# Performance work log

Hardware: AMD Instinct MI355X
Metric: run time of the kernel (lower is better)

The kernel has to match this reference:

```python
import jax, jax.numpy as jnp
import numpy as np
import math

D_MODEL = 1024
N_HEAD = 16          # sub-heads per branch
N_BR = 4             # hardcoded n_branches
DH = D_MODEL // N_HEAD
H_TOT = N_BR * N_HEAD
B, T = 1, 1024
SCALE = math.pi / math.sqrt(3.0)
ATTNSCALE = DH ** -0.5


def _rope(x):
    # x: [B, H, T, D]; matches torch RoPE: even/odd split, concat halves
    t_len, d = x.shape[2], x.shape[-1]
    inv_freq = 1.0 / (10000.0 ** (jnp.arange(0, d, 2, dtype=jnp.float32) / d))
    freqs = jnp.arange(t_len, dtype=jnp.float32)[:, None] * inv_freq[None, :]  # [T, D/2]
    cos, sin = jnp.cos(freqs), jnp.sin(freqs)
    x1, x2 = x[..., 0::2], x[..., 1::2]
    return jnp.concatenate([-x2 * sin + x1 * cos, x1 * sin + x2 * cos], axis=-1)


def setup_inputs() -> dict:
    key = jax.random.key(0)
    ks = jax.random.split(key, 12)
    s = D_MODEL ** -0.5
    return {
        "X": jax.random.normal(ks[0], (B, T, D_MODEL), jnp.float32),
        "W_Q": jax.random.normal(ks[1], (D_MODEL, D_MODEL * N_BR), jnp.float32) * s,
        "b_Q": jax.random.normal(ks[2], (D_MODEL * N_BR,), jnp.float32) * 0.02,
        "W_K": jax.random.normal(ks[3], (D_MODEL, D_MODEL), jnp.float32) * s,
        "b_K": jax.random.normal(ks[4], (D_MODEL,), jnp.float32) * 0.02,
        "W_V": jax.random.normal(ks[5], (D_MODEL, D_MODEL), jnp.float32) * s,
        "b_V": jax.random.normal(ks[6], (D_MODEL,), jnp.float32) * 0.02,
        "sink_scalars": jax.random.uniform(ks[7], (H_TOT,), jnp.float32, 0.0, 0.1),
        "v_nulls": jax.random.normal(ks[8], (N_BR, D_MODEL), jnp.float32) * 0.02,
        "W_O": jax.random.normal(ks[9], (N_BR, D_MODEL, D_MODEL), jnp.float32) * s,
        "W_O_bias": jax.random.normal(ks[10], (N_BR, D_MODEL), jnp.float32) * 0.02,
    }


def reference(X, W_Q, b_Q, W_K, b_K, W_V, b_V, sink_scalars, v_nulls, W_O, W_O_bias):
    Bv, Tv, C = X.shape
    # projections -> [B, H, T, Dh]
    q = (X @ W_Q + b_Q).reshape(Bv, Tv, H_TOT, DH).transpose(0, 2, 1, 3)
    k_base = (X @ W_K + b_K).reshape(Bv, Tv, N_HEAD, DH).transpose(0, 2, 1, 3)
    v_base = (X @ W_V + b_V).reshape(Bv, Tv, N_HEAD, DH).transpose(0, 2, 1, 3)
    k = jnp.tile(k_base, (1, N_BR, 1, 1))
    v = jnp.tile(v_base, (1, N_BR, 1, 1))
    q, k = _rope(q), _rope(k)

    scores = jnp.einsum("bhtd,bhsd->bhts", q, k) * ATTNSCALE
    key_self = jnp.clip(jnp.sum(k * k, axis=-1), 1e-6, None)      # [B,H,S]
    w = jax.nn.softplus(scores / jnp.sqrt(key_self)[:, :, None, :])
    causal = jnp.tril(jnp.ones((Tv, Tv), bool))                    # [T,S]
    w = jnp.where(causal, w, 0.0)
    w = w * jax.nn.sigmoid(SCALE * w)
    sinks = sink_scalars.reshape(1, H_TOT, 1, 1)
    w = jnp.where(w < sinks, 0.0, w)
    # concat-with-sink renormalization, expressed without the concat
    total = jnp.sum(w, axis=-1, keepdims=True) + sinks + 1e-6      # [B,H,T,1]
    probs_tokens = w / total
    probs_sink = sinks / total                                     # [B,H,T,1]

    out = jnp.einsum("bhts,bhsd->bhtd", probs_tokens, v)
    v_null = v_nulls.reshape(H_TOT, DH)[None, :, None, :]          # [1,H,1,Dh]
    out = out + probs_sink * v_null

    context = out.reshape(Bv, N_BR, N_HEAD, Tv, DH).transpose(0, 1, 3, 2, 4)
    context = context.reshape(Bv, N_BR, Tv, C)
    y = jnp.einsum("bntc,ncd->bntd", context, W_O) + W_O_bias[None, :, None, :]
    return y.mean(axis=1)
```

## Files before the change

kernel.cpp:

```cpp
#include <hip/hip_runtime.h>
#include <math.h>

typedef __attribute__((ext_vector_type(4))) float  f32x4;
typedef __attribute__((ext_vector_type(8))) short  bf16x8;
typedef __attribute__((ext_vector_type(4))) short  s16x4;

#define SQUISH_U 1.8137993642342178f
#define LN2F     0.69314718055994531f

__device__ __forceinline__ float b2f(short u) {
    union { float f; unsigned b; } v; v.b = ((unsigned)(unsigned short)u) << 16; return v.f;
}
__device__ __forceinline__ short f2b(float f) {
    union { float f; unsigned b; } v; v.f = f;
    unsigned r = (v.b + 0x7FFFu + ((v.b >> 16) & 1u)) >> 16;
    return (short)r;
}
__device__ __forceinline__ unsigned cvt_pk_bf16(float lo, float hi) {
    unsigned r;
    asm("v_cvt_pk_bf16_f32 %0, %1, %2" : "=v"(r) : "v"(lo), "v"(hi));
    return r;
}
__device__ __forceinline__ void gll16(const void* g, void* l) {
    __builtin_amdgcn_global_load_lds((const __attribute__((address_space(1))) void*)g,
                                     (__attribute__((address_space(3))) void*)l, 16, 0, 0);
}
__device__ __forceinline__ void gll4(const void* g, void* l) {
    __builtin_amdgcn_global_load_lds((const __attribute__((address_space(1))) void*)g,
                                     (__attribute__((address_space(3))) void*)l, 4, 0, 0);
}

__device__ __forceinline__ void do_transpose(const float* __restrict__ src, int R, int C,
                                             short* __restrict__ dst, float scale,
                                             int c0, int r0, float (*tile)[65], int tid) {
    #pragma unroll
    for (int it = 0; it < 4; ++it) {
        int lin = it * 256 + tid;
        int r = lin >> 4, c4 = lin & 15;
        f32x4 v = *(const f32x4*)(src + (size_t)(r0 + r) * C + c0 + c4 * 4);
        #pragma unroll
        for (int k = 0; k < 4; ++k) tile[r][c4 * 4 + k] = v[k];
    }
    __syncthreads();
    #pragma unroll
    for (int it = 0; it < 4; ++it) {
        int lin = it * 256 + tid;
        int c = lin >> 4, rq = lin & 15;
        s16x4 o;
        #pragma unroll
        for (int k = 0; k < 4; ++k) o[k] = f2b(tile[rq * 4 + k][c] * scale);
        *(s16x4*)(dst + (size_t)(c0 + c) * R + r0 + rq * 4) = o;
    }
}

__global__ __launch_bounds__(256) void prep_kernel(
    const float* __restrict__ X, const float* __restrict__ W_Q, const float* __restrict__ W_K,
    const float* __restrict__ W_V, const float* __restrict__ W_O,
    const float* __restrict__ bQ, const float* __restrict__ bK, const float* __restrict__ bV,
    const float* __restrict__ bO,
    short* __restrict__ Xb, short* __restrict__ WbT, short* __restrict__ WoT,
    float* __restrict__ biasQKV, float* __restrict__ out) {
    __shared__ float tile[64][65];
    const int bid = blockIdx.x, tid = threadIdx.x;
    if (bid < 256) {
        int i = (bid * 256 + tid) * 16;
        #pragma unroll
        for (int k = 0; k < 4; ++k) {
            f32x4 v = *(const f32x4*)(X + i + k * 4);
            s16x4 o;
            o.x = f2b(v.x); o.y = f2b(v.y); o.z = f2b(v.z); o.w = f2b(v.w);
            *(s16x4*)(Xb + i + k * 4) = o;
        }
    } else if (bid < 1280) {
        int b2 = bid - 256;
        do_transpose(W_Q, 1024, 4096, WbT, 1.f, (b2 & 63) * 64, (b2 >> 6) * 64, tile, tid);
    } else if (bid < 1536) {
        int b2 = bid - 1280;
        do_transpose(W_K, 1024, 1024, WbT + 4096 * 1024, 1.f, (b2 & 15) * 64, (b2 >> 4) * 64, tile, tid);
    } else if (bid < 1792) {
        int b2 = bid - 1536;
        do_transpose(W_V, 1024, 1024, WbT + 5120 * 1024, 1.f, (b2 & 15) * 64, (b2 >> 4) * 64, tile, tid);
    } else if (bid < 2816) {
        int b2 = bid - 1792;
        do_transpose(W_O, 4096, 1024, WoT, 0.25f, (b2 & 15) * 64, (b2 >> 4) * 64, tile, tid);
    } else if (bid < 2840) {
        int i = (bid - 2816) * 256 + tid;
        if (i < 4096)      biasQKV[i] = bQ[i];
        else if (i < 5120) biasQKV[i] = bK[i - 4096];
        else               biasQKV[i] = bV[i - 5120];
    } else {
        int i = ((bid - 2840) * 256 + tid) * 4;
        f32x4 v;
        #pragma unroll
        for (int k = 0; k < 4; ++k) {
            int c = (i + k) & 1023;
            v[k] = 0.25f * (bO[c] + bO[1024 + c] + bO[2048 + c] + bO[3072 + c]);
        }
        *(f32x4*)(out + i) = v;
    }
}

#define GSTAGE_64x128(k0_, b_) do {                                            \
    _Pragma("unroll")                                                          \
    for (int it = 0; it < 2; ++it) {                                           \
        int lin0 = it * 256 + wave * 64;                                       \
        int lin = lin0 + lane;                                                 \
        int r = lin >> 3, c = (lin & 7) ^ (r & 7);                             \
        gll16(A + (size_t)(m0 + r) * K + (k0_) + c * 8, (char*)lA[b_] + lin0 * 16); \
    }                                                                          \
    _Pragma("unroll")                                                          \
    for (int it = 0; it < 4; ++it) {                                           \
        int lin0 = it * 256 + wave * 64;                                       \
        int lin = lin0 + lane;                                                 \
        int r = lin >> 3, c = (lin & 7) ^ (r & 7);                             \
        gll16(BT + (size_t)(n0 + r) * K + (k0_) + c * 8, (char*)lB[b_] + lin0 * 16); \
    } } while (0)

#define GEMM_CORE_64x128(kbeg_, kend_)                                         \
    GSTAGE_64x128(kbeg_, 0);                                                   \
    int cur = 0;                                                               \
    for (int k0 = (kbeg_); k0 < (kend_); k0 += 64) {                           \
        if (k0 + 64 < (kend_)) {                                               \
            GSTAGE_64x128(k0 + 64, cur ^ 1);                                   \
            asm volatile("s_waitcnt vmcnt(6) lgkmcnt(0)" ::: "memory");        \
        } else {                                                               \
            asm volatile("s_waitcnt vmcnt(0) lgkmcnt(0)" ::: "memory");        \
        }                                                                      \
        __builtin_amdgcn_s_barrier();                                          \
        _Pragma("unroll")                                                      \
        for (int kk = 0; kk < 2; ++kk) {                                       \
            bf16x8 af[2], bf_[4];                                              \
            _Pragma("unroll")                                                  \
            for (int m = 0; m < 2; ++m) {                                      \
                int row = wr * 32 + m * 16 + l15;                              \
                int ch = (kk * 4 + l4) ^ (row & 7);                            \
                af[m] = *(const bf16x8*)&lA[cur][row][ch << 3];                \
            }                                                                  \
            _Pragma("unroll")                                                  \
            for (int n = 0; n < 4; ++n) {                                      \
                int row = wc * 64 + n * 16 + l15;                              \
                int ch = (kk * 4 + l4) ^ (row & 7);                            \
                bf_[n] = *(const bf16x8*)&lB[cur][row][ch << 3];               \
            }                                                                  \
            _Pragma("unroll")                                                  \
            for (int m = 0; m < 2; ++m)                                        \
                _Pragma("unroll")                                              \
                for (int n = 0; n < 4; ++n)                                    \
                    acc[m][n] = __builtin_amdgcn_mfma_f32_16x16x32_bf16(af[m], bf_[n], acc[m][n], 0, 0, 0); \
        }                                                                      \
        asm volatile("" ::: "memory");                                         \
        __builtin_amdgcn_s_barrier();                                          \
        cur ^= 1;                                                              \
    }

__global__ __launch_bounds__(256, 3) void gemm_qkv_kernel(
    const short* __restrict__ A, const short* __restrict__ BT,
    const float* __restrict__ bias, short* __restrict__ outB,
    int M, int N, int K) {
    __shared__ short lA[2][64][64];
    __shared__ short lB[2][128][64];
    const int tid = threadIdx.x;
    const int lane = tid & 63, wave = tid >> 6;
    const int l15 = lane & 15, l4 = lane >> 4;
    const int wr = wave >> 1, wc = wave & 1;
    const int n0 = blockIdx.x * 128, m0 = blockIdx.y * 64;

    f32x4 acc[2][4];
    const f32x4 fz = {0.f, 0.f, 0.f, 0.f};
    #pragma unroll
    for (int m = 0; m < 2; ++m)
        #pragma unroll
        for (int n = 0; n < 4; ++n) acc[m][n] = fz;

    GEMM_CORE_64x128(0, K);

    #pragma unroll
    for (int m = 0; m < 2; ++m)
        #pragma unroll
        for (int n = 0; n < 4; ++n)
            #pragma unroll
            for (int r = 0; r < 4; ++r) {
                int row = m0 + wr * 32 + m * 16 + l4 * 4 + r;
                int col = n0 + wc * 64 + n * 16 + l15;
                outB[(size_t)row * N + col] = f2b(acc[m][n][r] + bias[col]);
            }
}

__global__ __launch_bounds__(256, 3) void gemm_op_kernel(
    const short* __restrict__ A, const short* __restrict__ BT,
    float* __restrict__ out, int M, int N, int K, int KSLICE) {
    __shared__ short lA[2][64][64];
    __shared__ short lB[2][128][64];
    const int tid = threadIdx.x;
    const int lane = tid & 63, wave = tid >> 6;
    const int l15 = lane & 15, l4 = lane >> 4;
    const int wr = wave >> 1, wc = wave & 1;
    const int n0 = blockIdx.x * 128, m0 = blockIdx.y * 64;
    const int kbeg = blockIdx.z * KSLICE, kend = kbeg + KSLICE;

    f32x4 acc[2][4];
    const f32x4 fz = {0.f, 0.f, 0.f, 0.f};
    #pragma unroll
    for (int m = 0; m < 2; ++m)
        #pragma unroll
        for (int n = 0; n < 4; ++n) acc[m][n] = fz;

    GEMM_CORE_64x128(kbeg, kend);

    #pragma unroll
    for (int m = 0; m < 2; ++m)
        #pragma unroll
        for (int n = 0; n < 4; ++n)
            #pragma unroll
            for (int r = 0; r < 4; ++r) {
                int row = m0 + wr * 32 + m * 16 + l4 * 4 + r;
                int col = n0 + wc * 64 + n * 16 + l15;
                unsafeAtomicAdd(&out[(size_t)row * N + col], acc[m][n][r]);
            }
}

__global__ __launch_bounds__(256) void rope_vt_kernel(short* __restrict__ QKVb,
                                                      float* __restrict__ ksr,
                                                      short* __restrict__ Vtb) {
    __shared__ short tile[64][72];
    const int bid = blockIdx.x, tid = threadIdx.x;
    if (bid < 1280) {
        int base = bid * 256 + tid;
        #pragma unroll
        for (int it = 0; it < 8; ++it) {
            int item = base + it * 327680;
            int j = item & 31;
            int rem = item >> 5;
            int head = rem % 80;
            int t = rem / 80;
            short* p;
            if (head < 64) p = QKVb + (size_t)t * 6144 + head * 64;
            else           p = QKVb + (size_t)t * 6144 + 4096 + (head - 64) * 64;
            float x1 = b2f(p[2 * j]), x2 = b2f(p[2 * j + 1]);
            float freq = (float)t * __builtin_exp2f(-(float)j * 0.41524101186092033f);
            float sn = __sinf(freq), cs = __cosf(freq);
            float o1 = x1 * cs - x2 * sn;
            float o2 = x1 * sn + x2 * cs;
            p[j]      = f2b(o1);
            p[32 + j] = f2b(o2);
            if (head >= 64) {
                float ss = o1 * o1 + o2 * o2;
                #pragma unroll
                for (int off = 16; off; off >>= 1) ss += __shfl_xor(ss, off, 32);
                if (j == 0) ksr[(head - 64) * 1024 + t] = 0.18033688011112042f * rsqrtf(fmaxf(ss, 1e-6f));
            }
        }
    } else {
        int b2 = bid - 1280;
        int h = b2 >> 4, t0 = (b2 & 15) * 64;
        #pragma unroll
        for (int it = 0; it < 16; ++it) {
            int lin = it * 256 + tid;
            int r = lin >> 6, d = lin & 63;
            tile[r][d] = QKVb[(size_t)(t0 + r) * 6144 + 5120 + h * 64 + d];
        }
        __syncthreads();
        #pragma unroll
        for (int it = 0; it < 16; ++it) {
            int lin = it * 256 + tid;
            int d = lin >> 6, c = lin & 63;
            Vtb[(size_t)(h * 64 + d) * 1024 + t0 + c] = tile[c][d];
        }
    }
}

__constant__ __device__ const signed char TQT[24] = {15,15,14, 7,14,13,13,12, 6,12,11,11,10, 5,10, 9, 9, 8, 4, 8, 3, 2, 1, 0};
__constant__ __device__ const signed char TKB[24] = { 0, 8, 0, 0, 8, 0, 7, 0, 0, 7, 0, 6, 0, 0, 6, 0, 5, 0, 0, 5, 0, 0, 0, 0};
__constant__ __device__ const signed char TKE[24] = { 8,16, 8, 8,15, 7,14, 7, 7,13, 6,12, 6, 6,11, 5,10, 5, 5, 9, 4, 3, 2, 1};

__global__ __launch_bounds__(256, 6) void attn_kernel(
    const short* __restrict__ QKVb, const short* __restrict__ Vtb,
    const float* __restrict__ ksr, const float* __restrict__ sinks,
    const float* __restrict__ vnulls, short* __restrict__ Ob,
    float* __restrict__ Of, float* __restrict__ totf) {
    __shared__ short lK[64][64];
    __shared__ short lV[64][64];
    __shared__ float lks[64];
    __shared__ float lvn[64];
    __shared__ short lP[4][16][64];

    const int tid = threadIdx.x;
    const int lane = tid & 63, wave = tid >> 6;
    const int l15 = lane & 15, l4 = lane >> 4;
    const int h = blockIdx.x;
    const int slot = blockIdx.y;
    const int qt = TQT[slot], kb = TKB[slot], ke = TKE[slot];
    const bool single = (kb == 0) && (ke == qt + 1);
    const int h16 = h & 15;
    const int t0 = qt * 64;
    const float sink = sinks[h];
    if (tid < 64) lvn[tid] = vnulls[h * 64 + tid];

    const int q_abs = t0 + wave * 16 + l15;
    bf16x8 aq[2];
    #pragma unroll
    for (int kk = 0; kk < 2; ++kk)
        aq[kk] = *(const bf16x8*)(QKVb + (size_t)q_abs * 6144 + h * 64 + kk * 32 + l4 * 8);

    const f32x4 fz = {0.f, 0.f, 0.f, 0.f};
    f32x4 acc_o[4];
    #pragma unroll
    for (int n = 0; n < 4; ++n) acc_o[n] = fz;
    float tot = 0.f;

#define ASTAGE(s0_) do {                                                              \
    int lin0 = wave * 64;                                                             \
    int lin = lin0 + lane;                                                            \
    int r = lin >> 3, c = (lin & 7) ^ (r & 7);                                        \
    gll16(QKVb + (size_t)((s0_) + r) * 6144 + 4096 + h16 * 64 + c * 8, (char*)lK + lin0 * 16); \
    gll16(Vtb + (size_t)(h16 * 64 + r) * 1024 + (s0_) + c * 8,         (char*)lV + lin0 * 16); \
    lin0 += 256; lin = lin0 + lane; r = lin >> 3; c = (lin & 7) ^ (r & 7);            \
    gll16(QKVb + (size_t)((s0_) + r) * 6144 + 4096 + h16 * 64 + c * 8, (char*)lK + lin0 * 16); \
    gll16(Vtb + (size_t)(h16 * 64 + r) * 1024 + (s0_) + c * 8,         (char*)lV + lin0 * 16); \
    gll4(ksr + h16 * 1024 + (s0_) + lane, (char*)lks);                                \
} while (0)

    for (int kt = kb; kt < ke; ++kt) {
        int s0 = kt * 64;
        __syncthreads();
        ASTAGE(s0);
        asm volatile("s_waitcnt vmcnt(0)" ::: "memory");
        __syncthreads();

        f32x4 accs[4];
        #pragma unroll
        for (int n = 0; n < 4; ++n) accs[n] = fz;
        #pragma unroll
        for (int kk = 0; kk < 2; ++kk) {
            bf16x8 bk[4];
            #pragma unroll
            for (int n = 0; n < 4; ++n) {
                int row = n * 16 + l15;
                int ch = (kk * 4 + l4) ^ (row & 7);
                bk[n] = *(const bf16x8*)&lK[row][ch << 3];
            }
            #pragma unroll
            for (int n = 0; n < 4; ++n)
                accs[n] = __builtin_amdgcn_mfma_f32_16x16x32_bf16(bk[n], aq[kk], accs[n], 0, 0, 0);
        }

        #pragma unroll
        for (int n = 0; n < 4; ++n) {
            f32x4 ksv = *(const f32x4*)&lks[n * 16 + l4 * 4];
            float w4[4];
            #pragma unroll
            for (int r = 0; r < 4; ++r) {
                int k_abs = s0 + n * 16 + l4 * 4 + r;
                float zz = accs[n][r] * ksv[r];
                float t = __builtin_amdgcn_exp2f(zz);
                float u = __builtin_amdgcn_logf(1.f + t);
                u = (k_abs <= q_abs) ? u : 0.f;
                float g = __builtin_amdgcn_rcpf(1.f + __builtin_amdgcn_exp2f(-SQUISH_U * u));
                float w = LN2F * u * g;
                w = (w >= sink) ? w : 0.f;
                tot += w;
                w4[r] = w;
            }
            unsigned pa = cvt_pk_bf16(w4[0], w4[1]);
            unsigned pb = cvt_pk_bf16(w4[2], w4[3]);
            int ch = (2 * n + (l4 >> 1)) ^ (l15 & 7);
            uint2 val; val.x = pa; val.y = pb;
            *(uint2*)&lP[wave][l15][ch * 8 + (l4 & 1) * 4] = val;
        }

        #pragma unroll
        for (int kk = 0; kk < 2; ++kk) {
            bf16x8 ap = *(const bf16x8*)&lP[wave][l15][((kk * 4 + l4) ^ (l15 & 7)) << 3];
            bf16x8 bv[4];
            #pragma unroll
            for (int n = 0; n < 4; ++n) {
                int row = n * 16 + l15;
                int ch = (kk * 4 + l4) ^ (row & 7);
                bv[n] = *(const bf16x8*)&lV[row][ch << 3];
            }
            #pragma unroll
            for (int n = 0; n < 4; ++n)
                acc_o[n] = __builtin_amdgcn_mfma_f32_16x16x32_bf16(ap, bv[n], acc_o[n], 0, 0, 0);
        }
    }
#undef ASTAGE

    tot += __shfl_xor(tot, 16, 64);
    tot += __shfl_xor(tot, 32, 64);

    if (single) {
        float tq[4];
        #pragma unroll
        for (int r = 0; r < 4; ++r) tq[r] = __shfl(tot, l4 * 4 + r, 64);
        #pragma unroll
        for (int r = 0; r < 4; ++r) {
            float inv = __builtin_amdgcn_rcpf(tq[r] + sink + 1e-6f);
            int trow = t0 + wave * 16 + l4 * 4 + r;
            #pragma unroll
            for (int n = 0; n < 4; ++n) {
                int d = n * 16 + l15;
                float val = (acc_o[n][r] + sink * lvn[d]) * inv;
                Ob[(size_t)trow * 4096 + h * 64 + d] = f2b(val);
            }
        }
    } else {
        if (lane < 16)
            unsafeAtomicAdd(&totf[h * 512 + (t0 - 512) + wave * 16 + l15], tot);
        #pragma unroll
        for (int r = 0; r < 4; ++r) {
            int pr = h * 512 + (t0 - 512) + wave * 16 + l4 * 4 + r;
            #pragma unroll
            for (int n = 0; n < 4; ++n)
                unsafeAtomicAdd(&Of[(size_t)pr * 64 + n * 16 + l15], acc_o[n][r]);
        }
    }
}

__global__ __launch_bounds__(256) void norm_kernel(
    const float* __restrict__ Of, const float* __restrict__ totf,
    const float* __restrict__ sinks, const float* __restrict__ vnulls,
    short* __restrict__ Ob) {
    int gid = blockIdx.x * 256 + threadIdx.x;
    int i4 = gid * 4;
    int row = i4 >> 6;
    int d0 = i4 & 63;
    int h = row >> 9;
    int t = 512 + (row & 511);
    float sink = sinks[h];
    float inv = __builtin_amdgcn_rcpf(totf[row] + sink + 1e-6f);
    f32x4 o = *(const f32x4*)(Of + i4);
    s16x4 rs;
    #pragma unroll
    for (int k = 0; k < 4; ++k)
        rs[k] = f2b((o[k] + sink * vnulls[h * 64 + d0 + k]) * inv);
    *(s16x4*)(Ob + (size_t)t * 4096 + h * 64 + d0) = rs;
}

extern "C" void kernel_launch(void* const* d_in, const int* in_sizes, int n_in,
                              void* d_out, int out_size, void* d_ws, size_t ws_size,
                              hipStream_t stream) {
    const float* X        = (const float*)d_in[0];
    const float* W_Q      = (const float*)d_in[1];
    const float* b_Q      = (const float*)d_in[2];
    const float* W_K      = (const float*)d_in[3];
    const float* b_K      = (const float*)d_in[4];
    const float* W_V      = (const float*)d_in[5];
    const float* b_V      = (const float*)d_in[6];
    const float* sinks    = (const float*)d_in[7];
    const float* v_nulls  = (const float*)d_in[8];
    const float* W_O      = (const float*)d_in[9];
    const float* W_O_bias = (const float*)d_in[10];
    float* out = (float*)d_out;
    char* ws = (char*)d_ws;

    short* Xb        = (short*)(ws + 0);
    short* WbT       = (short*)(ws + 2097152);
    short* WoT       = (short*)(ws + 14680064);
    short* QKVb      = (short*)(ws + 23068672);
    short* Vtb       = (short*)(ws + 35651584);
    short* Ob        = (short*)(ws + 37748736);
    float* ksr       = (float*)(ws + 46137344);
    float* biasQKV   = (float*)(ws + 46202880);
    float* Of        = (float*)(ws + 2097152);
    float* totf      = Of + 64 * 512 * 64;

    prep_kernel<<<3864, 256, 0, stream>>>(X, W_Q, W_K, W_V, W_O, b_Q, b_K, b_V, W_O_bias,
                                          Xb, WbT, WoT, biasQKV, out);
    gemm_qkv_kernel<<<dim3(48, 16), 256, 0, stream>>>(Xb, WbT, biasQKV, QKVb, 1024, 6144, 1024);
    rope_vt_kernel<<<1536, 256, 0, stream>>>(QKVb, ksr, Vtb);
    hipMemsetAsync(Of, 0, (size_t)(64 * 512 * 64 + 64 * 512) * sizeof(float), stream);
    attn_kernel<<<dim3(64, 24), 256, 0, stream>>>(QKVb, Vtb, ksr, sinks, v_nulls, Ob, Of, totf);
    norm_kernel<<<2048, 256, 0, stream>>>(Of, totf, sinks, v_nulls, Ob);
    gemm_op_kernel<<<dim3(8, 16, 8), 256, 0, stream>>>(Ob, WoT, out, 1024, 1024, 4096, 512);
}
```

Measured before the change: 204.7 us.

## Fuse RoPE, key norms and V transpose into QKV GEMM epilogue; drop atomics

Moves RoPE, the key self-norm and the V transpose into the QKV GEMM epilogue, using lane shuffles within each 16-lane group to pair even and odd columns. This removes the separate rope_vt kernel and its extra read-modify-write pass over QKV. Attention split-K partials are now written to two separate buffers with plain stores instead of atomics, so the memset goes away and norm_kernel sums the two partials. The output GEMM split-K drops from 8 to 4 slices, which halves the atomic adds into the output at the cost of fewer, longer blocks.

```diff
diff --git a/kernel.cpp b/kernel.cpp
--- a/kernel.cpp
+++ b/kernel.cpp
@@ -153,9 +153,10 @@
         cur ^= 1;                                                              \
     }
 
-__global__ __launch_bounds__(256, 3) void gemm_qkv_kernel(
+__global__ __launch_bounds__(256, 3) void gemm_qkvf_kernel(
     const short* __restrict__ A, const short* __restrict__ BT,
-    const float* __restrict__ bias, short* __restrict__ outB,
+    const float* __restrict__ bias, short* __restrict__ QKVb,
+    short* __restrict__ Vtb, float* __restrict__ ksr,
     int M, int N, int K) {
     __shared__ short lA[2][64][64];
     __shared__ short lB[2][128][64];
@@ -174,16 +175,93 @@
 
     GEMM_CORE_64x128(0, K);
 
+    const int head = blockIdx.x * 2 + wc;
+    float bn[4];
+    #pragma unroll
+    for (int n = 0; n < 4; ++n) bn[n] = bias[head * 64 + n * 16 + l15];
     #pragma unroll
     for (int m = 0; m < 2; ++m)
         #pragma unroll
         for (int n = 0; n < 4; ++n)
+            #pragma unroll
+            for (int r = 0; r < 4; ++r) acc[m][n][r] += bn[n];
+
+    if (head < 80) {
+        const float invf0 = __builtin_exp2f(-(float)l15 * 0.41524101186092033f);
+        const float invf1 = invf0 * 0.01f;
+        const int p1 = (2 * l15) & 15, p2 = (2 * l15 + 1) & 15;
+        #pragma unroll
+        for (int m = 0; m < 2; ++m) {
+            int tb = m0 + wr * 32 + m * 16 + l4 * 4;
+            float x1lo[4], x2lo[4], x1hi[4], x2hi[4];
+            #pragma unroll
+            for (int r = 0; r < 4; ++r) {
+                float a0 = __shfl(acc[m][0][r], p1, 16), b0 = __shfl(acc[m][1][r], p1, 16);
+                float a1 = __shfl(acc[m][0][r], p2, 16), b1 = __shfl(acc[m][1][r], p2, 16);
+                x1lo[r] = (l15 < 8) ? a0 : b0;
+                x2lo[r] = (l15 < 8) ? a1 : b1;
+                float c0 = __shfl(acc[m][2][r], p1, 16), d0 = __shfl(acc[m][3][r], p1, 16);
+                float c1 = __shfl(acc[m][2][r], p2, 16), d1 = __shfl(acc[m][3][r], p2, 16);
+                x1hi[r] = (l15 < 8) ? c0 : d0;
+                x2hi[r] = (l15 < 8) ? c1 : d1;
+            }
+            #pragma unroll
+            for (int r = 0; r < 4; ++r) {
+                float tf = (float)(tb + r);
+                float f0 = tf * invf0, f1 = tf * invf1;
+                float s0 = __sinf(f0), c0 = __cosf(f0);
+                float s1 = __sinf(f1), c1 = __cosf(f1);
+                acc[m][0][r] = x1lo[r] * c0 - x2lo[r] * s0;
+                acc[m][2][r] = x1lo[r] * s0 + x2lo[r] * c0;
+                acc[m][1][r] = x1hi[r] * c1 - x2hi[r] * s1;
+                acc[m][3][r] = x1hi[r] * s1 + x2hi[r] * c1;
+            }
+        }
+    }
+
+    if (head >= 80) {
+        const int h16 = head - 80;
+        #pragma unroll
+        for (int m = 0; m < 2; ++m) {
+            int tb = m0 + wr * 32 + m * 16 + l4 * 4;
+            #pragma unroll
+            for (int n = 0; n < 4; ++n) {
+                s16x4 o;
+                #pragma unroll
+                for (int r = 0; r < 4; ++r) o[r] = f2b(acc[m][n][r]);
+                *(s16x4*)(Vtb + (size_t)(h16 * 64 + n * 16 + l15) * 1024 + tb) = o;
+            }
+        }
+    } else {
+        const size_t coff = (head < 64) ? (size_t)head * 64 : (size_t)(4096 + (head - 64) * 64);
+        #pragma unroll
+        for (int m = 0; m < 2; ++m)
             #pragma unroll
             for (int r = 0; r < 4; ++r) {
                 int row = m0 + wr * 32 + m * 16 + l4 * 4 + r;
-                int col = n0 + wc * 64 + n * 16 + l15;
-                outB[(size_t)row * N + col] = f2b(acc[m][n][r] + bias[col]);
-            }
+                #pragma unroll
+                for (int n = 0; n < 4; ++n)
+                    QKVb[(size_t)row * 6144 + coff + n * 16 + l15] = f2b(acc[m][n][r]);
+            }
+        if (head >= 64) {
+            const int h16 = head - 64;
+            #pragma unroll
+            for (int m = 0; m < 2; ++m)
+                #pragma unroll
+                for (int r = 0; r < 4; ++r) {
+                    float ss = 0.f;
+                    #pragma unroll
+                    for (int n = 0; n < 4; ++n) ss += acc[m][n][r] * acc[m][n][r];
+                    ss += __shfl_xor(ss, 1, 16);
+                    ss += __shfl_xor(ss, 2, 16);
+                    ss += __shfl_xor(ss, 4, 16);
+                    ss += __shfl_xor(ss, 8, 16);
+                    if (l15 == 0)
+                        ksr[h16 * 1024 + m0 + wr * 32 + m * 16 + l4 * 4 + r] =
+                            0.18033688011112042f * rsqrtf(fmaxf(ss, 1e-6f));
+                }
+        }
+    }
 }
 
 __global__ __launch_bounds__(256, 3) void gemm_op_kernel(
@@ -219,56 +297,6 @@
             }
 }
 
-__global__ __launch_bounds__(256) void rope_vt_kernel(short* __restrict__ QKVb,
-                                                      float* __restrict__ ksr,
-                                                      short* __restrict__ Vtb) {
-    __shared__ short tile[64][72];
-    const int bid = blockIdx.x, tid = threadIdx.x;
-    if (bid < 1280) {
-        int base = bid * 256 + tid;
-        #pragma unroll
-        for (int it = 0; it < 8; ++it) {
-            int item = base + it * 327680;
-            int j = item & 31;
-            int rem = item >> 5;
-            int head = rem % 80;
-            int t = rem / 80;
-            short* p;
-            if (head < 64) p = QKVb + (size_t)t * 6144 + head * 64;
-            else           p = QKVb + (size_t)t * 6144 + 4096 + (head - 64) * 64;
-            float x1 = b2f(p[2 * j]), x2 = b2f(p[2 * j + 1]);
-            float freq = (float)t * __builtin_exp2f(-(float)j * 0.41524101186092033f);
-            float sn = __sinf(freq), cs = __cosf(freq);
-            float o1 = x1 * cs - x2 * sn;
-            float o2 = x1 * sn + x2 * cs;
-            p[j]      = f2b(o1);
-            p[32 + j] = f2b(o2);
-            if (head >= 64) {
-                float ss = o1 * o1 + o2 * o2;
-                #pragma unroll
-                for (int off = 16; off; off >>= 1) ss += __shfl_xor(ss, off, 32);
-                if (j == 0) ksr[(head - 64) * 1024 + t] = 0.18033688011112042f * rsqrtf(fmaxf(ss, 1e-6f));
-            }
-        }
-    } else {
-        int b2 = bid - 1280;
-        int h = b2 >> 4, t0 = (b2 & 15) * 64;
-        #pragma unroll
-        for (int it = 0; it < 16; ++it) {
-            int lin = it * 256 + tid;
-            int r = lin >> 6, d = lin & 63;
-            tile[r][d] = QKVb[(size_t)(t0 + r) * 6144 + 5120 + h * 64 + d];
-        }
-        __syncthreads();
-        #pragma unroll
-        for (int it = 0; it < 16; ++it) {
-            int lin = it * 256 + tid;
-            int d = lin >> 6, c = lin & 63;
-            Vtb[(size_t)(h * 64 + d) * 1024 + t0 + c] = tile[c][d];
-        }
-    }
-}
-
 __constant__ __device__ const signed char TQT[24] = {15,15,14, 7,14,13,13,12, 6,12,11,11,10, 5,10, 9, 9, 8, 4, 8, 3, 2, 1, 0};
 __constant__ __device__ const signed char TKB[24] = { 0, 8, 0, 0, 8, 0, 7, 0, 0, 7, 0, 6, 0, 0, 6, 0, 5, 0, 0, 5, 0, 0, 0, 0};
 __constant__ __device__ const signed char TKE[24] = { 8,16, 8, 8,15, 7,14, 7, 7,13, 6,12, 6, 6,11, 5,10, 5, 5, 9, 4, 3, 2, 1};
@@ -277,7 +305,8 @@
     const short* __restrict__ QKVb, const short* __restrict__ Vtb,
     const float* __restrict__ ksr, const float* __restrict__ sinks,
     const float* __restrict__ vnulls, short* __restrict__ Ob,
-    float* __restrict__ Of, float* __restrict__ totf) {
+    float* __restrict__ Of0, float* __restrict__ Of1,
+    float* __restrict__ tot0, float* __restrict__ tot1) {
     __shared__ short lK[64][64];
     __shared__ short lV[64][64];
     __shared__ float lks[64];
@@ -404,20 +433,22 @@
             }
         }
     } else {
-        if (lane < 16)
-            unsafeAtomicAdd(&totf[h * 512 + (t0 - 512) + wave * 16 + l15], tot);
+        float* Op = (kb == 0) ? Of0 : Of1;
+        float* tp = (kb == 0) ? tot0 : tot1;
+        if (lane < 16) tp[h * 512 + (t0 - 512) + wave * 16 + l15] = tot;
         #pragma unroll
         for (int r = 0; r < 4; ++r) {
             int pr = h * 512 + (t0 - 512) + wave * 16 + l4 * 4 + r;
             #pragma unroll
             for (int n = 0; n < 4; ++n)
-                unsafeAtomicAdd(&Of[(size_t)pr * 64 + n * 16 + l15], acc_o[n][r]);
+                Op[(size_t)pr * 64 + n * 16 + l15] = acc_o[n][r];
         }
     }
 }
 
 __global__ __launch_bounds__(256) void norm_kernel(
-    const float* __restrict__ Of, const float* __restrict__ totf,
+    const float* __restrict__ Of0, const float* __restrict__ Of1,
+    const float* __restrict__ tot0, const float* __restrict__ tot1,
     const float* __restrict__ sinks, const float* __restrict__ vnulls,
     short* __restrict__ Ob) {
     int gid = blockIdx.x * 256 + threadIdx.x;
@@ -427,12 +458,13 @@
     int h = row >> 9;
     int t = 512 + (row & 511);
     float sink = sinks[h];
-    float inv = __builtin_amdgcn_rcpf(totf[row] + sink + 1e-6f);
-    f32x4 o = *(const f32x4*)(Of + i4);
+    float inv = __builtin_amdgcn_rcpf(tot0[row] + tot1[row] + sink + 1e-6f);
+    f32x4 a = *(const f32x4*)(Of0 + i4);
+    f32x4 b = *(const f32x4*)(Of1 + i4);
     s16x4 rs;
     #pragma unroll
     for (int k = 0; k < 4; ++k)
-        rs[k] = f2b((o[k] + sink * vnulls[h * 64 + d0 + k]) * inv);
+        rs[k] = f2b((a[k] + b[k] + sink * vnulls[h * 64 + d0 + k]) * inv);
     *(s16x4*)(Ob + (size_t)t * 4096 + h * 64 + d0) = rs;
 }
 
@@ -461,15 +493,17 @@
     short* Ob        = (short*)(ws + 37748736);
     float* ksr       = (float*)(ws + 46137344);
     float* biasQKV   = (float*)(ws + 46202880);
-    float* Of        = (float*)(ws + 2097152);
-    float* totf      = Of + 64 * 512 * 64;
+    float* Of0       = (float*)(ws + 50331648);
+    float* Of1       = (float*)(ws + 58720256);
+    float* tot0      = (float*)(ws + 67108864);
+    float* tot1      = (float*)(ws + 67239936);
 
     prep_kernel<<<3864, 256, 0, stream>>>(X, W_Q, W_K, W_V, W_O, b_Q, b_K, b_V, W_O_bias,
                                           Xb, WbT, WoT, biasQKV, out);
-    gemm_qkv_kernel<<<dim3(48, 16), 256, 0, stream>>>(Xb, WbT, biasQKV, QKVb, 1024, 6144, 1024);
-    rope_vt_kernel<<<1536, 256, 0, stream>>>(QKVb, ksr, Vtb);
-    hipMemsetAsync(Of, 0, (size_t)(64 * 512 * 64 + 64 * 512) * sizeof(float), stream);
-    attn_kernel<<<dim3(64, 24), 256, 0, stream>>>(QKVb, Vtb, ksr, sinks, v_nulls, Ob, Of, totf);
-    norm_kernel<<<2048, 256, 0, stream>>>(Of, totf, sinks, v_nulls, Ob);
-    gemm_op_kernel<<<dim3(8, 16, 8), 256, 0, stream>>>(Ob, WoT, out, 1024, 1024, 4096, 512);
-}
+    gemm_qkvf_kernel<<<dim3(48, 16), 256, 0, stream>>>(Xb, WbT, biasQKV, QKVb, Vtb, ksr,
+                                                       1024, 6144, 1024);
+    attn_kernel<<<dim3(64, 24), 256, 0, stream>>>(QKVb, Vtb, ksr, sinks, v_nulls, Ob,
+                                                  Of0, Of1, tot0, tot1);
+    norm_kernel<<<2048, 256, 0, stream>>>(Of0, Of1, tot0, tot1, sinks, v_nulls, Ob);
+    gemm_op_kernel<<<dim3(8, 16, 4), 256, 0, stream>>>(Ob, WoT, out, 1024, 1024, 4096, 1024);
+}
```

After: 184.4 us. -9.9%, faster.
